# Optimization experiments

Measured on AMD Instinct MI355X. Metric: run time of the kernel, lower is better.

Reference implementation:

```python
import math
import jax, jax.numpy as jnp
import numpy as np

B, L, D = 2, 2048, 2048
H, DH = 16, 128
DFF = 8192


def setup_inputs() -> dict:
    key = jax.random.key(0)
    ks = jax.random.split(key, 9)
    x = jax.random.normal(ks[0], (B, L, D), dtype=jnp.float32)
    # additive causal mask: 0 on/below diagonal, -inf above
    neg = jnp.finfo(jnp.float32).min
    mask = jnp.where(jnp.tril(jnp.ones((L, L), dtype=bool)), 0.0, neg)[None, None]
    s = 0.02
    return {
        "x": x,
        "mask": mask,
        "ln1_w": jnp.ones((D,), jnp.float32),
        "wq": jax.random.normal(ks[1], (D, D), jnp.float32) * s,
        "wk": jax.random.normal(ks[2], (D, D), jnp.float32) * s,
        "wv": jax.random.normal(ks[3], (D, D), jnp.float32) * s,
        "wo": jax.random.normal(ks[4], (D, D), jnp.float32) * s,
        "ln2_w": jnp.ones((D,), jnp.float32),
        "w_up": jax.random.normal(ks[5], (DFF, D), jnp.float32) * s,
        "w_down": jax.random.normal(ks[6], (D, DFF), jnp.float32) * s,
    }


def _rmsnorm(x, w, eps=1e-8):
    rms = jnp.sqrt(jnp.mean(x * x, axis=-1, keepdims=True) + eps)
    return x / rms * w


def reference(x, mask, ln1_w, wq, wk, wv, wo, ln2_w, w_up, w_down):
    h = _rmsnorm(x, ln1_w)
    # torch Linear: y = x @ W.T ; weights are [out, in]
    q = (h @ wq.T).reshape(B, L, H, DH).transpose(0, 2, 1, 3)  # [B,H,L,DH]
    k = (h @ wk.T).reshape(B, L, H, DH).transpose(0, 2, 1, 3)
    v = (h @ wv.T).reshape(B, L, H, DH).transpose(0, 2, 1, 3)
    scores = jnp.einsum('bhqd,bhkd->bhqk', q, k) / math.sqrt(DH)
    scores = scores + mask
    attn = jax.nn.softmax(scores, axis=-1)
    out = jnp.einsum('bhqk,bhkd->bhqd', attn, v)
    out = out.transpose(0, 2, 1, 3).reshape(B, L, D)
    x = x + out @ wo.T
    h = _rmsnorm(x, ln2_w)
    ff = jax.nn.gelu(h @ w_up.T, approximate=False) @ w_down.T  # exact erf GELU as in F.gelu
    return x + ff
```

## Files before the change

### kernel.cpp

```cpp
#include <hip/hip_runtime.h>
#include <hip/hip_bf16.h>
#include <math.h>

#define B_   2
#define L_   2048
#define D_   2048
#define H_   16
#define DH_  128
#define DFF_ 8192
#define NTOK (B_*L_)

typedef __attribute__((ext_vector_type(8))) short bf16x8;
typedef __attribute__((ext_vector_type(4))) float floatx4;
typedef unsigned short u16;

__device__ __forceinline__ u16 f2bf(float f) {
    union { float f; unsigned u; } c; c.f = f;
    unsigned r = (c.u + 0x7fffu + ((c.u >> 16) & 1u)) >> 16;
    return (u16)r;
}

__device__ __forceinline__ void async_cp16(const u16* g, u16* l) {
    __builtin_amdgcn_global_load_lds(
        (const __attribute__((address_space(1))) unsigned int*)g,
        (__attribute__((address_space(3))) unsigned int*)l,
        16, 0, 0);
}

__global__ __launch_bounds__(256) void cvt_bf16(const float* __restrict__ in,
                                                u16* __restrict__ out, int n4) {
    int i = blockIdx.x * 256 + threadIdx.x;
    if (i >= n4) return;
    float4 v = ((const float4*)in)[i];
    ushort4 o = { f2bf(v.x), f2bf(v.y), f2bf(v.z), f2bf(v.w) };
    ((ushort4*)out)[i] = o;
}

__global__ __launch_bounds__(256) void rmsnorm_kernel(const float* __restrict__ x,
                                                      const float* __restrict__ w,
                                                      u16* __restrict__ out) {
    const int row = blockIdx.x, tid = threadIdx.x;
    const float* xr = x + (size_t)row * D_;
    float4 a = ((const float4*)xr)[tid];
    float4 b = ((const float4*)xr)[tid + 256];
    float ss = a.x*a.x + a.y*a.y + a.z*a.z + a.w*a.w
             + b.x*b.x + b.y*b.y + b.z*b.z + b.w*b.w;
#pragma unroll
    for (int d = 1; d < 64; d <<= 1) ss += __shfl_xor(ss, d, 64);
    __shared__ float sred[4];
    if ((tid & 63) == 0) sred[tid >> 6] = ss;
    __syncthreads();
    float tot = sred[0] + sred[1] + sred[2] + sred[3];
    float inv = 1.0f / sqrtf(tot * (1.0f / D_) + 1e-8f);
    float4 w0 = ((const float4*)w)[tid];
    float4 w1 = ((const float4*)w)[tid + 256];
    ushort4 o0 = { f2bf(a.x*inv*w0.x), f2bf(a.y*inv*w0.y), f2bf(a.z*inv*w0.z), f2bf(a.w*inv*w0.w) };
    ushort4 o1 = { f2bf(b.x*inv*w1.x), f2bf(b.y*inv*w1.y), f2bf(b.z*inv*w1.z), f2bf(b.w*inv*w1.w) };
    ushort4* orow = (ushort4*)(out + (size_t)row * D_);
    orow[tid] = o0;
    orow[tid + 256] = o1;
}

template<int MODE>
__global__ __launch_bounds__(256) void gemm_bt(const u16* __restrict__ A,
                                               const u16* __restrict__ Bw,
                                               void* __restrict__ outp,
                                               void* __restrict__ outp2,
                                               const float* __restrict__ residual,
                                               int M, int N, int K, float scale) {
    __shared__ __attribute__((aligned(16))) u16 lds_a[2][128 * 32];
    __shared__ __attribute__((aligned(16))) u16 lds_b[2][128 * 32];
    const int tid = threadIdx.x;
    const int wave = tid >> 6, lane = tid & 63;
    const int qd = lane >> 4, c16 = lane & 15;
    const int wm = (wave >> 1) * 64, wn = (wave & 1) * 64;
    const long tile_m = (long)blockIdx.y * 128, tile_n = (long)blockIdx.x * 128;

    floatx4 acc[4][4] = {};

    const int r0 = tid >> 2;
    const int r1 = r0 + 64;
    const int kc = (tid & 3) * 8;
    const u16* a0 = A + (tile_m + r0) * (long)K + kc;
    const u16* a1 = A + (tile_m + r1) * (long)K + kc;
    const u16* b0 = Bw + (tile_n + r0) * (long)K + kc;
    const u16* b1 = Bw + (tile_n + r1) * (long)K + kc;

    for (int k0 = 0; k0 < K; k0 += 64) {
#pragma unroll
        for (int p = 0; p < 2; p++) {
            const int kp = k0 + p * 32;
            async_cp16(a0 + kp, &lds_a[p][r0 * 32 + kc]);
            async_cp16(a1 + kp, &lds_a[p][r1 * 32 + kc]);
            async_cp16(b0 + kp, &lds_b[p][r0 * 32 + kc]);
            async_cp16(b1 + kp, &lds_b[p][r1 * 32 + kc]);
        }
        __syncthreads();
#pragma unroll
        for (int p = 0; p < 2; p++) {
            bf16x8 af[4], bv[4];
#pragma unroll
            for (int i = 0; i < 4; i++)
                af[i] = *(const bf16x8*)&lds_a[p][(wm + i * 16 + c16) * 32 + qd * 8];
#pragma unroll
            for (int j = 0; j < 4; j++)
                bv[j] = *(const bf16x8*)&lds_b[p][(wn + j * 16 + c16) * 32 + qd * 8];
#pragma unroll
            for (int i = 0; i < 4; i++)
#pragma unroll
                for (int j = 0; j < 4; j++)
                    acc[i][j] = __builtin_amdgcn_mfma_f32_16x16x32_bf16(af[i], bv[j], acc[i][j], 0, 0, 0);
        }
        __syncthreads();
    }

#pragma unroll
    for (int i = 0; i < 4; i++) {
#pragma unroll
        for (int j = 0; j < 4; j++) {
#pragma unroll
            for (int r = 0; r < 4; r++) {
                long m = tile_m + wm + i * 16 + qd * 4 + r;
                long n = tile_n + wn + j * 16 + c16;
                float v = acc[i][j][r];
                if (MODE == 0) {
                    long b = m >> 11, l = m & 2047;
                    int isq = n < D_;
                    long f = n & 2047, h = f >> 7, dh = f & 127;
                    u16* dst = isq ? (u16*)outp : (u16*)outp2;
                    dst[((b * H_ + h) * (long)L_ + l) * DH_ + dh] =
                        f2bf(v * (isq ? scale : 1.0f));
                } else if (MODE == 1) {
                    long idx = m * (long)N + n;
                    ((float*)outp)[idx] = v + residual[idx];
                } else if (MODE == 2) {
                    float g = 0.5f * v * (1.0f + erff(v * 0.70710678118654752f));
                    ((u16*)outp)[m * (long)N + n] = f2bf(g);
                } else {
                    ((u16*)outp)[m * (long)N + n] = f2bf(v);
                }
            }
        }
    }
}

#define KSTRIDE 136
#define VSTRIDE 72
#define PSTRIDE 72
__global__ __launch_bounds__(256) void attn_kernel(const u16* __restrict__ Q,
                                                   const u16* __restrict__ K,
                                                   const u16* __restrict__ VT,
                                                   u16* __restrict__ O) {
    __shared__ __attribute__((aligned(16))) u16 kt_lds[64 * KSTRIDE];
    __shared__ __attribute__((aligned(16))) u16 vt_lds[128 * VSTRIDE];
    __shared__ __attribute__((aligned(16))) u16 p_lds[4][16 * PSTRIDE];
    const int tid = threadIdx.x;
    const int wave = tid >> 6, lane = tid & 63;
    const int qd = lane >> 4, c16 = lane & 15;
    const int pair = blockIdx.x, bh = blockIdx.y;
    const int b = bh >> 4, h = bh & 15;
    const u16* qh = Q + (size_t)bh * L_ * DH_;
    const u16* kh = K + (size_t)bh * L_ * DH_;
    const u16* vth = VT + (size_t)h * DH_ * NTOK + (size_t)b * L_;

    for (int qsel = 0; qsel < 2; ++qsel) {
        const int qt = qsel ? (31 - pair) : pair;
        const int q0 = qt * 64;

        bf16x8 qf[4];
#pragma unroll
        for (int s = 0; s < 4; s++)
            qf[s] = *(const bf16x8*)(qh + (size_t)(q0 + wave * 16 + c16) * DH_ + s * 32 + qd * 8);

        floatx4 o_acc[8] = {};
        float m_i[4], l_i[4];
#pragma unroll
        for (int r = 0; r < 4; r++) { m_i[r] = -1e30f; l_i[r] = 0.f; }

        for (int kt = 0; kt <= qt; kt++) {
            const int kv0 = kt * 64;
#pragma unroll
            for (int s = 0; s < 4; s++) {
                int c = tid + s * 256;
                int kr = c >> 4, koff = (c & 15) * 8;
                *(int4*)&kt_lds[kr * KSTRIDE + koff] =
                    *(const int4*)(kh + (size_t)(kv0 + kr) * DH_ + koff);
                int dh = c >> 3, kv8 = (c & 7) * 8;
                *(int4*)&vt_lds[dh * VSTRIDE + kv8] =
                    *(const int4*)(vth + (size_t)dh * NTOK + kv0 + kv8);
            }
            __syncthreads();

            floatx4 s_acc[4] = {};
#pragma unroll
            for (int j = 0; j < 4; j++)
#pragma unroll
                for (int s = 0; s < 4; s++) {
                    bf16x8 kf = *(const bf16x8*)&kt_lds[(j * 16 + c16) * KSTRIDE + s * 32 + qd * 8];
                    s_acc[j] = __builtin_amdgcn_mfma_f32_16x16x32_bf16(qf[s], kf, s_acc[j], 0, 0, 0);
                }

            if (kt == qt) {
#pragma unroll
                for (int j = 0; j < 4; j++)
#pragma unroll
                    for (int r = 0; r < 4; r++) {
                        int col = j * 16 + c16;
                        int row = wave * 16 + qd * 4 + r;
                        if (col > row) s_acc[j][r] = -1e30f;
                    }
            }

            float rsum[4], alpha[4];
#pragma unroll
            for (int r = 0; r < 4; r++) {
                float mx = fmaxf(fmaxf(s_acc[0][r], s_acc[1][r]), fmaxf(s_acc[2][r], s_acc[3][r]));
#pragma unroll
                for (int d = 1; d < 16; d <<= 1) mx = fmaxf(mx, __shfl_xor(mx, d, 64));
                float mnew = fmaxf(m_i[r], mx);
                alpha[r] = __expf(m_i[r] - mnew);
                m_i[r] = mnew;
                rsum[r] = 0.f;
            }
#pragma unroll
            for (int j = 0; j < 4; j++)
#pragma unroll
                for (int r = 0; r < 4; r++) {
                    float p = __expf(s_acc[j][r] - m_i[r]);
                    s_acc[j][r] = p;
                    rsum[r] += p;
                }
#pragma unroll
            for (int r = 0; r < 4; r++) {
#pragma unroll
                for (int d = 1; d < 16; d <<= 1) rsum[r] += __shfl_xor(rsum[r], d, 64);
                l_i[r] = l_i[r] * alpha[r] + rsum[r];
            }
#pragma unroll
            for (int j8 = 0; j8 < 8; j8++)
#pragma unroll
                for (int r = 0; r < 4; r++) o_acc[j8][r] *= alpha[r];

#pragma unroll
            for (int j = 0; j < 4; j++)
#pragma unroll
                for (int r = 0; r < 4; r++)
                    p_lds[wave][(qd * 4 + r) * PSTRIDE + j * 16 + c16] = f2bf(s_acc[j][r]);

#pragma unroll
            for (int s = 0; s < 2; s++) {
                bf16x8 pf = *(const bf16x8*)&p_lds[wave][c16 * PSTRIDE + s * 32 + qd * 8];
#pragma unroll
                for (int j8 = 0; j8 < 8; j8++) {
                    bf16x8 vf = *(const bf16x8*)&vt_lds[(j8 * 16 + c16) * VSTRIDE + s * 32 + qd * 8];
                    o_acc[j8] = __builtin_amdgcn_mfma_f32_16x16x32_bf16(pf, vf, o_acc[j8], 0, 0, 0);
                }
            }
            __syncthreads();
        }

        float inv_l[4];
#pragma unroll
        for (int r = 0; r < 4; r++) inv_l[r] = 1.0f / l_i[r];
#pragma unroll
        for (int j8 = 0; j8 < 8; j8++)
#pragma unroll
            for (int r = 0; r < 4; r++) {
                int l = q0 + wave * 16 + qd * 4 + r;
                int d = h * DH_ + j8 * 16 + c16;
                O[(size_t)(b * L_ + l) * D_ + d] = f2bf(o_acc[j8][r] * inv_l[r]);
            }
    }
}

extern "C" void kernel_launch(void* const* d_in, const int* in_sizes, int n_in,
                              void* d_out, int out_size, void* d_ws, size_t ws_size,
                              hipStream_t stream) {
    const float* x     = (const float*)d_in[0];
    const float* ln1_w = (const float*)d_in[2];
    const float* wq    = (const float*)d_in[3];
    const float* wk    = (const float*)d_in[4];
    const float* wv    = (const float*)d_in[5];
    const float* wo    = (const float*)d_in[6];
    const float* ln2_w = (const float*)d_in[7];
    const float* w_up  = (const float*)d_in[8];
    const float* w_dn  = (const float*)d_in[9];

    char* ws = (char*)d_ws;
    const size_t MB = 1024 * 1024;
    float* x2   = (float*)(ws + 0);
    u16* hbuf   = (u16*)(ws + 32 * MB);
    u16* qbuf   = (u16*)(ws + 48 * MB);
    u16* kbuf   = (u16*)(ws + 64 * MB);
    u16* vtbuf  = (u16*)(ws + 80 * MB);
    u16* attnb  = (u16*)(ws + 96 * MB);
    u16* upbuf  = (u16*)(ws + 48 * MB);
    u16* wbufA  = (u16*)(ws + 112 * MB);
    u16* wbufC  = (u16*)(ws + 128 * MB);

    dim3 blk(256);
    const int nW = D_ * D_;
    const int nU = DFF_ * D_;
    cvt_bf16<<<(nW / 4 + 255) / 256, blk, 0, stream>>>(wq, wbufA, nW / 4);
    cvt_bf16<<<(nW / 4 + 255) / 256, blk, 0, stream>>>(wk, wbufA + (size_t)nW, nW / 4);
    cvt_bf16<<<(nW / 4 + 255) / 256, blk, 0, stream>>>(wv, wbufC, nW / 4);
    rmsnorm_kernel<<<NTOK, blk, 0, stream>>>(x, ln1_w, hbuf);

    dim3 gqk(2 * D_ / 128, NTOK / 128);
    gemm_bt<0><<<gqk, blk, 0, stream>>>(hbuf, wbufA, qbuf, kbuf, nullptr,
                                        NTOK, 2 * D_, D_, 0.08838834764831845f);
    dim3 gv(NTOK / 128, D_ / 128);
    gemm_bt<3><<<gv, blk, 0, stream>>>(wbufC, hbuf, vtbuf, nullptr, nullptr, D_, NTOK, D_, 1.0f);

    dim3 ga(16, B_ * H_);
    attn_kernel<<<ga, blk, 0, stream>>>(qbuf, kbuf, vtbuf, attnb);

    cvt_bf16<<<(nW / 4 + 255) / 256, blk, 0, stream>>>(wo, wbufA, nW / 4);
    dim3 g1(D_ / 128, NTOK / 128);
    gemm_bt<1><<<g1, blk, 0, stream>>>(attnb, wbufA, x2, nullptr, x, NTOK, D_, D_, 1.0f);

    rmsnorm_kernel<<<NTOK, blk, 0, stream>>>(x2, ln2_w, hbuf);

    cvt_bf16<<<(nU / 4 + 255) / 256, blk, 0, stream>>>(w_up, wbufA, nU / 4);
    dim3 g2(DFF_ / 128, NTOK / 128);
    gemm_bt<2><<<g2, blk, 0, stream>>>(hbuf, wbufA, upbuf, nullptr, nullptr, NTOK, DFF_, D_, 1.0f);

    cvt_bf16<<<(nU / 4 + 255) / 256, blk, 0, stream>>>(w_dn, wbufA, nU / 4);
    gemm_bt<1><<<g1, blk, 0, stream>>>(upbuf, wbufA, (float*)d_out, nullptr, x2, NTOK, D_, DFF_, 1.0f);
}
```

Before: 871.0 us.

## Replace 128x128 GEMM with swizzled, software-pipelined 256x256 tile kernel

Every bf16 GEMM now uses a new 512-thread kernel with 256x256 output tiles, a 64-wide K step, XOR-swizzled LDS layout and a double-buffered async global-to-LDS pipeline. Loads for upcoming K tiles are interleaved between MFMA groups, with explicit vmcnt/lgkmcnt waits, barriers and s_setprio to keep the matrix units fed. The aim is more data reuse per block, fewer LDS bank conflicts and less exposed memory latency than the old kernel, which synchronised on every step. In exchange, each block uses about 128KB of LDS, so only one block fits per CU. The D-output GEMMs (wo, down projection) now launch only 128 blocks, which can leave many CUs idle.

```diff
diff --git a/kernel.cpp b/kernel.cpp
--- a/kernel.cpp
+++ b/kernel.cpp
@@ -62,66 +62,109 @@
 }
 
 template<int MODE>
-__global__ __launch_bounds__(256) void gemm_bt(const u16* __restrict__ A,
-                                               const u16* __restrict__ Bw,
-                                               void* __restrict__ outp,
-                                               void* __restrict__ outp2,
-                                               const float* __restrict__ residual,
-                                               int M, int N, int K, float scale) {
-    __shared__ __attribute__((aligned(16))) u16 lds_a[2][128 * 32];
-    __shared__ __attribute__((aligned(16))) u16 lds_b[2][128 * 32];
+__global__ __launch_bounds__(512, 2) void gemm256(const u16* __restrict__ A,
+                                                  const u16* __restrict__ Bw,
+                                                  void* __restrict__ outp,
+                                                  void* __restrict__ outp2,
+                                                  const float* __restrict__ residual,
+                                                  int M, int N, int K, float scale) {
+    __shared__ __attribute__((aligned(16))) u16 lds_a[2][256 * 64];
+    __shared__ __attribute__((aligned(16))) u16 lds_b[2][256 * 64];
     const int tid = threadIdx.x;
     const int wave = tid >> 6, lane = tid & 63;
     const int qd = lane >> 4, c16 = lane & 15;
-    const int wm = (wave >> 1) * 64, wn = (wave & 1) * 64;
-    const long tile_m = (long)blockIdx.y * 128, tile_n = (long)blockIdx.x * 128;
-
-    floatx4 acc[4][4] = {};
-
-    const int r0 = tid >> 2;
-    const int r1 = r0 + 64;
-    const int kc = (tid & 3) * 8;
-    const u16* a0 = A + (tile_m + r0) * (long)K + kc;
-    const u16* a1 = A + (tile_m + r1) * (long)K + kc;
-    const u16* b0 = Bw + (tile_n + r0) * (long)K + kc;
-    const u16* b1 = Bw + (tile_n + r1) * (long)K + kc;
-
-    for (int k0 = 0; k0 < K; k0 += 64) {
-#pragma unroll
-        for (int p = 0; p < 2; p++) {
-            const int kp = k0 + p * 32;
-            async_cp16(a0 + kp, &lds_a[p][r0 * 32 + kc]);
-            async_cp16(a1 + kp, &lds_a[p][r1 * 32 + kc]);
-            async_cp16(b0 + kp, &lds_b[p][r0 * 32 + kc]);
-            async_cp16(b1 + kp, &lds_b[p][r1 * 32 + kc]);
-        }
-        __syncthreads();
-#pragma unroll
-        for (int p = 0; p < 2; p++) {
-            bf16x8 af[4], bv[4];
-#pragma unroll
-            for (int i = 0; i < 4; i++)
-                af[i] = *(const bf16x8*)&lds_a[p][(wm + i * 16 + c16) * 32 + qd * 8];
-#pragma unroll
-            for (int j = 0; j < 4; j++)
-                bv[j] = *(const bf16x8*)&lds_b[p][(wn + j * 16 + c16) * 32 + qd * 8];
-#pragma unroll
-            for (int i = 0; i < 4; i++)
-#pragma unroll
-                for (int j = 0; j < 4; j++)
-                    acc[i][j] = __builtin_amdgcn_mfma_f32_16x16x32_bf16(af[i], bv[j], acc[i][j], 0, 0, 0);
-        }
-        __syncthreads();
+    const int wm = wave >> 2, wn = wave & 3;
+    const long tile_m = (long)blockIdx.y * 256, tile_n = (long)blockIdx.x * 256;
+    const int NT = K >> 6;
+
+    const int srow = tid >> 3;
+    const int scol = ((tid & 7) * 8) ^ (((tid >> 5) & 1) << 4);
+    const u16* Asrc = A + (tile_m + srow) * (long)K + scol;
+    const u16* Bsrc = Bw + (tile_n + srow) * (long)K + scol;
+    const int stoff = tid * 8;
+
+#define STAGE_A2(bi, g0, g1, ko) do { \
+        async_cp16(Asrc + (long)(g0) * 64 * K + (ko), &lds_a[bi][(g0) * 4096 + stoff]); \
+        async_cp16(Asrc + (long)(g1) * 64 * K + (ko), &lds_a[bi][(g1) * 4096 + stoff]); \
+    } while (0)
+#define STAGE_B2(bi, g0, g1, ko) do { \
+        async_cp16(Bsrc + (long)(g0) * 64 * K + (ko), &lds_b[bi][(g0) * 4096 + stoff]); \
+        async_cp16(Bsrc + (long)(g1) * 64 * K + (ko), &lds_b[bi][(g1) * 4096 + stoff]); \
+    } while (0)
+
+    const int swz = (c16 & 4) << 3;
+    const int abase = (((wm * 128 + c16) * 128 + qd * 16) ^ swz);
+    const int bbase = (((wn * 64 + c16) * 128 + qd * 16) ^ swz);
+#define LDAF(bi, i, ks) (*(const bf16x8*)((const char*)&lds_a[bi][0] + abase + (i) * 2048 + (ks) * 64))
+#define LDBF(bi, j, ks) (*(const bf16x8*)((const char*)&lds_b[bi][0] + bbase + (j) * 2048 + (ks) * 64))
+#define MFMA_(a, b, c) __builtin_amdgcn_mfma_f32_16x16x32_bf16(a, b, c, 0, 0, 0)
+
+    floatx4 acc[8][4] = {};
+
+    STAGE_B2(0, 0, 1, 0); STAGE_B2(0, 2, 3, 0);
+    STAGE_A2(0, 0, 2, 0); STAGE_A2(0, 1, 3, 0);
+    STAGE_B2(1, 0, 1, 64); STAGE_B2(1, 2, 3, 64);
+    STAGE_A2(1, 0, 2, 64);
+    asm volatile("s_waitcnt vmcnt(6)" ::: "memory");
+    __builtin_amdgcn_s_barrier();
+    asm volatile("" ::: "memory");
+
+    bf16x8 bfr[4][2];
+
+#define GP(bi, ip, STAGE, TAIL) do { \
+        bf16x8 a0k0 = LDAF(bi, 2 * (ip), 0); \
+        bf16x8 a0k1 = LDAF(bi, 2 * (ip), 1); \
+        bf16x8 a1k0 = LDAF(bi, 2 * (ip) + 1, 0); \
+        bf16x8 a1k1 = LDAF(bi, 2 * (ip) + 1, 1); \
+        STAGE \
+        __builtin_amdgcn_s_barrier(); \
+        asm volatile("s_waitcnt lgkmcnt(0)" ::: "memory"); \
+        __builtin_amdgcn_sched_barrier(0); \
+        __builtin_amdgcn_s_setprio(1); \
+        _Pragma("unroll") \
+        for (int j = 0; j < 4; j++) { \
+            acc[2 * (ip)][j]     = MFMA_(a0k0, bfr[j][0], acc[2 * (ip)][j]); \
+            acc[2 * (ip)][j]     = MFMA_(a0k1, bfr[j][1], acc[2 * (ip)][j]); \
+            acc[2 * (ip) + 1][j] = MFMA_(a1k0, bfr[j][0], acc[2 * (ip) + 1][j]); \
+            acc[2 * (ip) + 1][j] = MFMA_(a1k1, bfr[j][1], acc[2 * (ip) + 1][j]); \
+        } \
+        __builtin_amdgcn_s_setprio(0); \
+        __builtin_amdgcn_sched_barrier(0); \
+        TAIL \
+        __builtin_amdgcn_s_barrier(); \
+        asm volatile("" ::: "memory"); \
+    } while (0)
+
+#define VMTAIL { if (s2) asm volatile("s_waitcnt vmcnt(6)" ::: "memory"); \
+                 else    asm volatile("s_waitcnt vmcnt(0)" ::: "memory"); }
+
+    for (int t = 0; t < NT; t += 2) {
+        const int s2 = (t + 2) < NT;
+        const long ko1 = (long)(t + 1) * 64;
+        const long ko2 = (long)(t + 2) * 64;
+        const long ko3 = (long)(t + 3) * 64;
+#pragma unroll
+        for (int j = 0; j < 4; j++) { bfr[j][0] = LDBF(0, j, 0); bfr[j][1] = LDBF(0, j, 1); }
+        GP(0, 0, STAGE_A2(1, 1, 3, ko1);, );
+        GP(0, 1, if (s2) STAGE_B2(0, 0, 1, ko2);, );
+        GP(0, 2, if (s2) STAGE_B2(0, 2, 3, ko2);, );
+        GP(0, 3, if (s2) STAGE_A2(0, 0, 2, ko2);, VMTAIL);
+#pragma unroll
+        for (int j = 0; j < 4; j++) { bfr[j][0] = LDBF(1, j, 0); bfr[j][1] = LDBF(1, j, 1); }
+        GP(1, 0, if (s2) STAGE_A2(0, 1, 3, ko2);, );
+        GP(1, 1, if (s2) STAGE_B2(1, 0, 1, ko3);, );
+        GP(1, 2, if (s2) STAGE_B2(1, 2, 3, ko3);, );
+        GP(1, 3, if (s2) STAGE_A2(1, 0, 2, ko3);, VMTAIL);
     }
 
 #pragma unroll
-    for (int i = 0; i < 4; i++) {
+    for (int i = 0; i < 8; i++) {
 #pragma unroll
         for (int j = 0; j < 4; j++) {
 #pragma unroll
             for (int r = 0; r < 4; r++) {
-                long m = tile_m + wm + i * 16 + qd * 4 + r;
-                long n = tile_n + wn + j * 16 + c16;
+                long m = tile_m + wm * 128 + i * 16 + qd * 4 + r;
+                long n = tile_n + wn * 64 + j * 16 + c16;
                 float v = acc[i][j][r];
                 if (MODE == 0) {
                     long b = m >> 11, l = m & 2047;
@@ -142,6 +185,13 @@
             }
         }
     }
+#undef GP
+#undef VMTAIL
+#undef STAGE_A2
+#undef STAGE_B2
+#undef LDAF
+#undef LDBF
+#undef MFMA_
 }
 
 #define KSTRIDE 136
@@ -298,7 +348,7 @@
     u16* wbufA  = (u16*)(ws + 112 * MB);
     u16* wbufC  = (u16*)(ws + 128 * MB);
 
-    dim3 blk(256);
+    dim3 blk(256), blk512(512);
     const int nW = D_ * D_;
     const int nU = DFF_ * D_;
     cvt_bf16<<<(nW / 4 + 255) / 256, blk, 0, stream>>>(wq, wbufA, nW / 4);
@@ -306,25 +356,25 @@
     cvt_bf16<<<(nW / 4 + 255) / 256, blk, 0, stream>>>(wv, wbufC, nW / 4);
     rmsnorm_kernel<<<NTOK, blk, 0, stream>>>(x, ln1_w, hbuf);
 
-    dim3 gqk(2 * D_ / 128, NTOK / 128);
-    gemm_bt<0><<<gqk, blk, 0, stream>>>(hbuf, wbufA, qbuf, kbuf, nullptr,
-                                        NTOK, 2 * D_, D_, 0.08838834764831845f);
-    dim3 gv(NTOK / 128, D_ / 128);
-    gemm_bt<3><<<gv, blk, 0, stream>>>(wbufC, hbuf, vtbuf, nullptr, nullptr, D_, NTOK, D_, 1.0f);
+    gemm256<0><<<dim3(2 * D_ / 256, NTOK / 256), blk512, 0, stream>>>(
+        hbuf, wbufA, qbuf, kbuf, nullptr, NTOK, 2 * D_, D_, 0.08838834764831845f);
+    gemm256<3><<<dim3(NTOK / 256, D_ / 256), blk512, 0, stream>>>(
+        wbufC, hbuf, vtbuf, nullptr, nullptr, D_, NTOK, D_, 1.0f);
 
     dim3 ga(16, B_ * H_);
     attn_kernel<<<ga, blk, 0, stream>>>(qbuf, kbuf, vtbuf, attnb);
 
     cvt_bf16<<<(nW / 4 + 255) / 256, blk, 0, stream>>>(wo, wbufA, nW / 4);
-    dim3 g1(D_ / 128, NTOK / 128);
-    gemm_bt<1><<<g1, blk, 0, stream>>>(attnb, wbufA, x2, nullptr, x, NTOK, D_, D_, 1.0f);
+    gemm256<1><<<dim3(D_ / 256, NTOK / 256), blk512, 0, stream>>>(
+        attnb, wbufA, x2, nullptr, x, NTOK, D_, D_, 1.0f);
 
     rmsnorm_kernel<<<NTOK, blk, 0, stream>>>(x2, ln2_w, hbuf);
 
     cvt_bf16<<<(nU / 4 + 255) / 256, blk, 0, stream>>>(w_up, wbufA, nU / 4);
-    dim3 g2(DFF_ / 128, NTOK / 128);
-    gemm_bt<2><<<g2, blk, 0, stream>>>(hbuf, wbufA, upbuf, nullptr, nullptr, NTOK, DFF_, D_, 1.0f);
+    gemm256<2><<<dim3(DFF_ / 256, NTOK / 256), blk512, 0, stream>>>(
+        hbuf, wbufA, upbuf, nullptr, nullptr, NTOK, DFF_, D_, 1.0f);
 
     cvt_bf16<<<(nU / 4 + 255) / 256, blk, 0, stream>>>(w_dn, wbufA, nU / 4);
-    gemm_bt<1><<<g1, blk, 0, stream>>>(upbuf, wbufA, (float*)d_out, nullptr, x2, NTOK, D_, DFF_, 1.0f);
-}
+    gemm256<1><<<dim3(D_ / 256, NTOK / 256), blk512, 0, stream>>>(
+        upbuf, wbufA, (float*)d_out, nullptr, x2, NTOK, D_, DFF_, 1.0f);
+}
```

Measured after the change: 1.031 ms. 18.4% more time.
